# Kernel optimization log

Measured on AMD Instinct MI355X. Metric: run time of the kernel, lower is better.

Reference implementation:

```python
import jax, jax.numpy as jnp
import numpy as np

EPS = 1e-12  # matches torch F.normalize default eps


def _normalize(x):
    n = jnp.linalg.norm(x, axis=-1, keepdims=True)
    return x / jnp.maximum(n, EPS)


def _time_interp(t, e, L, E):
    """linear_interpolation_time: [B] t,e; L:[m] landmarks; E:[m,m] emb table."""
    m = L.shape[0]
    idx = jnp.searchsorted(L, t)              # torch.searchsorted, side='left'
    idx = jnp.where(idx == 0, 1, idx)
    idx = jnp.where(idx == m, m - 1, idx)
    E_hi, E_lo = E[idx], E[idx - 1]           # [B, m]
    L_hi, L_lo = L[idx], L[idx - 1]           # [B]
    coef = (E_hi - E_lo) / (L_hi - L_lo)[:, None]
    out = E_lo + coef * (t - L_lo)[:, None]
    # censor mask row i: mean of landmark embeddings j >= idx[i]
    denom = (m - idx).astype(E.dtype)[:, None]
    mask = (jnp.arange(m)[None, :] >= idx[:, None]).astype(E.dtype) / denom  # [B, m]
    out_censor = mask @ E.T                   # [B, m]
    e = e[:, None]
    return (out * e + out_censor * (1.0 - e)).astype(jnp.float32)


def setup_inputs() -> dict:
    key = jax.random.key(0)
    B, m = 8192, 256
    k_z, k_t, k_e = jax.random.split(key, 3)
    z = jax.random.normal(k_z, (B, m), dtype=jnp.float32)
    t = jax.random.uniform(k_t, (B,), dtype=jnp.float32, minval=0.0, maxval=10.0)
    e = (jax.random.uniform(k_e, (B,)) < 0.7).astype(jnp.float32)
    log_tau = jnp.zeros((1,), dtype=jnp.float32)            # tau=1.0 -> log 1 = 0
    time_landmark = jnp.linspace(0.0, 10.0, m, dtype=jnp.float32)
    time_emb_landmark = jnp.eye(m, dtype=jnp.float32)        # learnable eye init
    return {"z": z, "t": t, "e": e, "log_tau": log_tau,
            "time_emb_landmark": time_emb_landmark, "time_landmark": time_landmark}


def reference(z, t, e, log_tau, time_emb_landmark, time_landmark):
    B = z.shape[0]
    tau = jnp.sqrt(jnp.exp(log_tau))                         # [1]
    hz = _normalize(z) / tau                                  # enc = Identity
    hy = _normalize(_time_interp(t, e, time_landmark, time_emb_landmark)) / tau
    sim = hz @ hy.T                                           # [B, B]
    g = jnp.diagonal(sim)[:, None]                            # positives [B,1]
    # off-diagonal logits g0 - g: mask diagonal with -inf (exp -> 0 in logsumexp)
    eye = jnp.eye(B, dtype=bool)
    logits = jnp.where(eye, -jnp.inf, sim - g)
    slogits = jax.nn.logsumexp(logits, axis=1, keepdims=True)  # [B,1]
    # CrossEntropyLoss(sim, arange) per row = logsumexp(sim) - sim[i,i]
    dummy_ce = (jax.nn.logsumexp(sim, axis=1, keepdims=True) - g) - jnp.log(
        jnp.float32(B))
    out = jax.lax.stop_gradient(dummy_ce) + jnp.exp(
        slogits - jax.lax.stop_gradient(slogits)) - 1.0
    return jnp.clip(out, -5.0, 15.0)                          # [B,1]
```

## Files before the change

kernel.cpp:

```cpp
#include <hip/hip_runtime.h>
#include <hip/hip_bf16.h>

using short8 = __attribute__((ext_vector_type(8))) short;
using f32x4  = __attribute__((ext_vector_type(4))) float;

#define BM 128
#define BN 128
#define BK 64

__device__ inline void gload_lds16(const void* g, void* lds) {
    __builtin_amdgcn_global_load_lds(
        (const __attribute__((address_space(1))) void*)g,
        (__attribute__((address_space(3))) void*)lds, 16, 0, 0);
}

__global__ __launch_bounds__(256) void suffix_kernel(const float* __restrict__ E,
                                                     float* __restrict__ ST, int m) {
    int j = blockIdx.x;
    int k = threadIdx.x;
    int lane = k & 63, w = k >> 6;
    __shared__ float wtot[4];
    float v = (k < m) ? E[(size_t)j * m + k] : 0.f;
    #pragma unroll
    for (int off = 1; off < 64; off <<= 1) {
        float o = __shfl_down(v, off);
        if (lane + off < 64) v += o;
    }
    if (lane == 0) wtot[w] = v;
    __syncthreads();
    float add = 0.f;
    #pragma unroll
    for (int w2 = 0; w2 < 4; ++w2)
        if (w2 > w) add += wtot[w2];
    v += add;
    if (k < m) ST[(size_t)k * m + j] = v;
}

__global__ __launch_bounds__(256) void prep_kernel(
    const float* __restrict__ z, const float* __restrict__ t,
    const float* __restrict__ e, const float* __restrict__ log_tau,
    const float* __restrict__ E, const float* __restrict__ L,
    const float* __restrict__ ST,
    __hip_bfloat16* __restrict__ hz, __hip_bfloat16* __restrict__ hy,
    float* __restrict__ g, float* __restrict__ acc, int B, int m)
{
    int row  = blockIdx.x * 4 + (threadIdx.x >> 6);
    int lane = threadIdx.x & 63;
    if (row >= B) return;

    float tv = t[row], ev = e[row];

    int lo = 0, hi = m;
    while (lo < hi) { int mid = (lo + hi) >> 1; if (L[mid] < tv) lo = mid + 1; else hi = mid; }
    int idx = lo;
    if (idx == 0) idx = 1;
    if (idx == m) idx = m - 1;

    float Llo = L[idx - 1], Lhi = L[idx];
    float w    = (tv - Llo) / (Lhi - Llo);
    float invd = 1.0f / (float)(m - idx);
    float tau  = sqrtf(expf(log_tau[0]));
    float invtau = 1.0f / tau;

    int j0 = lane * 4;
    f32x4 zz = *(const f32x4*)&z[(size_t)row * m + j0];
    f32x4 El = *(const f32x4*)&E[(size_t)(idx - 1) * m + j0];
    f32x4 Eh = *(const f32x4*)&E[(size_t)idx * m + j0];
    f32x4 Sc = *(const f32x4*)&ST[(size_t)idx * m + j0];

    float yv[4];
    float ssy = 0.f, ssz = 0.f;
    #pragma unroll
    for (int p = 0; p < 4; ++p) {
        float yint = El[p] + (Eh[p] - El[p]) * w;
        float ycen = Sc[p] * invd;
        float y = yint * ev + ycen * (1.f - ev);
        yv[p] = y; ssy += y * y;
        ssz += zz[p] * zz[p];
    }
    #pragma unroll
    for (int off = 1; off < 64; off <<= 1) {
        ssy += __shfl_xor(ssy, off);
        ssz += __shfl_xor(ssz, off);
    }
    float sy = invtau / fmaxf(sqrtf(ssy), 1e-12f);
    float sz = invtau / fmaxf(sqrtf(ssz), 1e-12f);

    float gp = 0.f;
    ushort uy[4], uz[4];
    #pragma unroll
    for (int p = 0; p < 4; ++p) {
        float hyv = yv[p] * sy, hzv = zz[p] * sz;
        gp += hyv * hzv;
        __hip_bfloat16 hb = __float2bfloat16(hyv);
        __hip_bfloat16 zb = __float2bfloat16(hzv);
        uy[p] = *reinterpret_cast<unsigned short*>(&hb);
        uz[p] = *reinterpret_cast<unsigned short*>(&zb);
    }
    *(ushort4*)&hy[(size_t)row * m + j0] = make_ushort4(uy[0], uy[1], uy[2], uy[3]);
    *(ushort4*)&hz[(size_t)row * m + j0] = make_ushort4(uz[0], uz[1], uz[2], uz[3]);
    #pragma unroll
    for (int off = 1; off < 64; off <<= 1) gp += __shfl_xor(gp, off);
    if (lane == 0) { g[row] = gp; acc[row] = 0.f; }
}

__global__ __launch_bounds__(256, 2) void gemm_lse_kernel(
    const __hip_bfloat16* __restrict__ hz, const __hip_bfloat16* __restrict__ hy,
    float* __restrict__ row_acc, int B, int K)
{
    __shared__ __hip_bfloat16 As[2][BM * BK];
    __shared__ __hip_bfloat16 Bs[2][BN * BK];

    const int tid  = threadIdx.x;
    const int wv   = tid >> 6;
    const int lane = tid & 63;
    const int wr   = wv >> 1;
    const int wc   = wv & 1;

    int bx = blockIdx.x, by = blockIdx.y;
    {
        int nx = gridDim.x, ny = gridDim.y;
        int nwg = nx * ny;
        if ((nwg & 7) == 0 && ny >= 8) {
            int orig = by * nx + bx;
            int xcd = orig & 7;
            int pos = orig >> 3;
            by = (xcd << 3) | (pos & 7);
            bx = pos >> 3;
        }
    }
    const int row0 = by * BM;
    const int col0 = bx * BN;

    f32x4 acc[4][4];
    #pragma unroll
    for (int i = 0; i < 4; ++i)
        #pragma unroll
        for (int j = 0; j < 4; ++j)
            acc[i][j] = (f32x4){0.f, 0.f, 0.f, 0.f};

    const int l8 = lane >> 3;
    const int c8 = lane & 7;

    const int nkb = K / BK;

#define STAGE(buf, kb)                                                          \
    do {                                                                        \
        _Pragma("unroll")                                                       \
        for (int p = 0; p < 4; ++p) {                                           \
            int r  = p * 32 + wv * 8 + l8;                                      \
            int cg = c8 ^ (r & 7);                                              \
            gload_lds16(hz + (size_t)(row0 + r) * K + (kb) * BK + cg * 8,       \
                        (void*)&As[buf][(p * 32 + wv * 8) * BK]);               \
            gload_lds16(hy + (size_t)(col0 + r) * K + (kb) * BK + cg * 8,       \
                        (void*)&Bs[buf][(p * 32 + wv * 8) * BK]);               \
        }                                                                       \
    } while (0)

    STAGE(0, 0);

    for (int kb = 0; kb < nkb; ++kb) {
        const int cur = kb & 1;
        asm volatile("" ::: "memory");
        if (kb + 1 < nkb) {
            STAGE(cur ^ 1, kb + 1);
            asm volatile("s_waitcnt vmcnt(8)" ::: "memory");
        } else {
            asm volatile("s_waitcnt vmcnt(0)" ::: "memory");
        }
        __builtin_amdgcn_s_barrier();

        const int lm = lane & 15, lk = lane >> 4;
        #pragma unroll
        for (int kk = 0; kk < 2; ++kk) {
            short8 a[4], b[4];
            #pragma unroll
            for (int mi = 0; mi < 4; ++mi) {
                int rt = wr * 64 + mi * 16 + lm;
                int cs = (kk * 4 + lk) ^ (rt & 7);
                a[mi] = *(const short8*)&As[cur][rt * BK + cs * 8];
            }
            #pragma unroll
            for (int ni = 0; ni < 4; ++ni) {
                int rt = wc * 64 + ni * 16 + lm;
                int cs = (kk * 4 + lk) ^ (rt & 7);
                b[ni] = *(const short8*)&Bs[cur][rt * BK + cs * 8];
            }
            #pragma unroll
            for (int mi = 0; mi < 4; ++mi)
                #pragma unroll
                for (int ni = 0; ni < 4; ++ni)
                    acc[mi][ni] = __builtin_amdgcn_mfma_f32_16x16x32_bf16(
                        a[mi], b[ni], acc[mi][ni], 0, 0, 0);
        }
        __builtin_amdgcn_s_barrier();
    }
#undef STAGE

    const int lm = lane & 15, lg = lane >> 4;
    #pragma unroll
    for (int mi = 0; mi < 4; ++mi) {
        float rs[4] = {0.f, 0.f, 0.f, 0.f};
        #pragma unroll
        for (int ni = 0; ni < 4; ++ni) {
            #pragma unroll
            for (int r = 0; r < 4; ++r) rs[r] += __expf(acc[mi][ni][r]);
        }
        #pragma unroll
        for (int r = 0; r < 4; ++r) {
            float s = rs[r];
            s += __shfl_xor(s, 1);
            s += __shfl_xor(s, 2);
            s += __shfl_xor(s, 4);
            s += __shfl_xor(s, 8);
            if (lm == 0)
                unsafeAtomicAdd(&row_acc[row0 + wr * 64 + mi * 16 + lg * 4 + r], s);
        }
    }
}

__global__ void finalize_kernel(const float* __restrict__ acc, const float* __restrict__ g,
                                float* __restrict__ out, int B) {
    int i = blockIdx.x * 256 + threadIdx.x;
    if (i < B) {
        float v = logf(acc[i]) - g[i] - logf((float)B);
        out[i] = fminf(fmaxf(v, -5.f), 15.f);
    }
}

extern "C" void kernel_launch(void* const* d_in, const int* in_sizes, int n_in,
                              void* d_out, int out_size, void* d_ws, size_t ws_size,
                              hipStream_t stream) {
    const float* z       = (const float*)d_in[0];
    const float* t       = (const float*)d_in[1];
    const float* e       = (const float*)d_in[2];
    const float* log_tau = (const float*)d_in[3];
    const float* E       = (const float*)d_in[4];
    const float* L       = (const float*)d_in[5];
    float* out = (float*)d_out;

    const int B = in_sizes[1];
    const int m = in_sizes[5];

    char* w = (char*)d_ws;
    __hip_bfloat16* hz = (__hip_bfloat16*)w;
    __hip_bfloat16* hy = hz + (size_t)B * m;
    float* ST  = (float*)(hy + (size_t)B * m);
    float* g   = ST + (size_t)m * m;
    float* acc = g + B;

    suffix_kernel<<<m, 256, 0, stream>>>(E, ST, m);
    prep_kernel<<<B / 4, 256, 0, stream>>>(z, t, e, log_tau, E, L, ST, hz, hy, g, acc, B, m);
    dim3 grid2(B / BN, B / BM);
    gemm_lse_kernel<<<grid2, 256, 0, stream>>>(hz, hy, acc, B, m);
    finalize_kernel<<<(B + 255) / 256, 256, 0, stream>>>(acc, g, out, B);
}
```

Measured before the change: 141.8 us.

## Enlarge GEMM tile to 256x256 with 8 waves and interleaved staged prefetch

```diff
diff --git a/kernel.cpp b/kernel.cpp
--- a/kernel.cpp
+++ b/kernel.cpp
@@ -4,9 +4,10 @@
 using short8 = __attribute__((ext_vector_type(8))) short;
 using f32x4  = __attribute__((ext_vector_type(4))) float;
 
-#define BM 128
-#define BN 128
+#define BM 256
+#define BN 256
 #define BK 64
+#define NKT 4
 
 __device__ inline void gload_lds16(const void* g, void* lds) {
     __builtin_amdgcn_global_load_lds(
@@ -104,102 +105,137 @@
     if (lane == 0) { g[row] = gp; acc[row] = 0.f; }
 }
 
-__global__ __launch_bounds__(256, 2) void gemm_lse_kernel(
+__global__ __launch_bounds__(512, 2) void gemm_lse_kernel(
     const __hip_bfloat16* __restrict__ hz, const __hip_bfloat16* __restrict__ hy,
-    float* __restrict__ row_acc, int B, int K)
+    float* __restrict__ row_acc, int Brows, int K)
 {
     __shared__ __hip_bfloat16 As[2][BM * BK];
     __shared__ __hip_bfloat16 Bs[2][BN * BK];
 
     const int tid  = threadIdx.x;
-    const int wv   = tid >> 6;
+    const int wid  = tid >> 6;
     const int lane = tid & 63;
-    const int wr   = wv >> 1;
-    const int wc   = wv & 1;
+    const int wm   = wid >> 2;
+    const int wn   = wid & 3;
 
     int bx = blockIdx.x, by = blockIdx.y;
-    {
-        int nx = gridDim.x, ny = gridDim.y;
-        int nwg = nx * ny;
-        if ((nwg & 7) == 0 && ny >= 8) {
-            int orig = by * nx + bx;
-            int xcd = orig & 7;
-            int pos = orig >> 3;
-            by = (xcd << 3) | (pos & 7);
-            bx = pos >> 3;
-        }
-    }
-    const int row0 = by * BM;
-    const int col0 = bx * BN;
-
-    f32x4 acc[4][4];
-    #pragma unroll
-    for (int i = 0; i < 4; ++i)
+    if (gridDim.x == 32 && gridDim.y == 32) {
+        int orig = by * 32 + bx;
+        int xcd = orig & 7, pos = orig >> 3;
+        by = (xcd << 2) | (pos & 3);
+        bx = pos >> 2;
+    }
+    const int row0 = by * BM, col0 = bx * BN;
+
+    f32x4 acc[8][4];
+    #pragma unroll
+    for (int i = 0; i < 8; ++i)
         #pragma unroll
         for (int j = 0; j < 4; ++j)
             acc[i][j] = (f32x4){0.f, 0.f, 0.f, 0.f};
 
-    const int l8 = lane >> 3;
-    const int c8 = lane & 7;
-
-    const int nkb = K / BK;
-
-#define STAGE(buf, kb)                                                          \
+    const int srow = tid >> 3;
+    const int c8   = tid & 7;
+    const int cg   = c8 ^ (srow & 7);
+    const int lm   = lane & 15, lk = lane >> 4;
+
+#define STAGE_A(buf, kt)                                                        \
     do {                                                                        \
         _Pragma("unroll")                                                       \
-        for (int p = 0; p < 4; ++p) {                                           \
-            int r  = p * 32 + wv * 8 + l8;                                      \
-            int cg = c8 ^ (r & 7);                                              \
-            gload_lds16(hz + (size_t)(row0 + r) * K + (kb) * BK + cg * 8,       \
-                        (void*)&As[buf][(p * 32 + wv * 8) * BK]);               \
-            gload_lds16(hy + (size_t)(col0 + r) * K + (kb) * BK + cg * 8,       \
-                        (void*)&Bs[buf][(p * 32 + wv * 8) * BK]);               \
-        }                                                                       \
+        for (int s = 0; s < 4; ++s)                                             \
+            gload_lds16(hz + (size_t)(row0 + s * 64 + srow) * K + (kt) * BK + cg * 8, \
+                        (void*)&As[buf][s * 4096 + wid * 512]);                 \
     } while (0)
-
-    STAGE(0, 0);
-
-    for (int kb = 0; kb < nkb; ++kb) {
-        const int cur = kb & 1;
-        asm volatile("" ::: "memory");
-        if (kb + 1 < nkb) {
-            STAGE(cur ^ 1, kb + 1);
-            asm volatile("s_waitcnt vmcnt(8)" ::: "memory");
-        } else {
-            asm volatile("s_waitcnt vmcnt(0)" ::: "memory");
-        }
-        __builtin_amdgcn_s_barrier();
-
-        const int lm = lane & 15, lk = lane >> 4;
-        #pragma unroll
-        for (int kk = 0; kk < 2; ++kk) {
-            short8 a[4], b[4];
-            #pragma unroll
-            for (int mi = 0; mi < 4; ++mi) {
-                int rt = wr * 64 + mi * 16 + lm;
-                int cs = (kk * 4 + lk) ^ (rt & 7);
-                a[mi] = *(const short8*)&As[cur][rt * BK + cs * 8];
-            }
-            #pragma unroll
-            for (int ni = 0; ni < 4; ++ni) {
-                int rt = wc * 64 + ni * 16 + lm;
-                int cs = (kk * 4 + lk) ^ (rt & 7);
-                b[ni] = *(const short8*)&Bs[cur][rt * BK + cs * 8];
-            }
-            #pragma unroll
-            for (int mi = 0; mi < 4; ++mi)
-                #pragma unroll
-                for (int ni = 0; ni < 4; ++ni)
-                    acc[mi][ni] = __builtin_amdgcn_mfma_f32_16x16x32_bf16(
-                        a[mi], b[ni], acc[mi][ni], 0, 0, 0);
-        }
-        __builtin_amdgcn_s_barrier();
-    }
-#undef STAGE
-
-    const int lm = lane & 15, lg = lane >> 4;
-    #pragma unroll
-    for (int mi = 0; mi < 4; ++mi) {
+#define STAGE_B(buf, kt)                                                        \
+    do {                                                                        \
+        _Pragma("unroll")                                                       \
+        for (int s = 0; s < 4; ++s)                                             \
+            gload_lds16(hy + (size_t)(col0 + s * 64 + srow) * K + (kt) * BK + cg * 8, \
+                        (void*)&Bs[buf][s * 4096 + wid * 512]);                 \
+    } while (0)
+
+#define LDSA(buf, rt, q) (*(const short8*)&As[buf][(rt) * BK + ((q) ^ ((rt) & 7)) * 8])
+#define LDSB(buf, rt, q) (*(const short8*)&Bs[buf][(rt) * BK + ((q) ^ ((rt) & 7)) * 8])
+
+    STAGE_A(0, 0);
+    STAGE_B(0, 0);
+    asm volatile("s_waitcnt vmcnt(0)" ::: "memory");
+    __builtin_amdgcn_s_barrier();
+
+    #pragma unroll
+    for (int kt = 0; kt < NKT; ++kt) {
+        const int cur = kt & 1, nxt = cur ^ 1;
+        short8 a[4], b[4];
+
+        #pragma unroll
+        for (int mi = 0; mi < 4; ++mi)
+            a[mi] = LDSA(cur, wm * 128 + mi * 16 + lm, lk);
+        #pragma unroll
+        for (int ni = 0; ni < 4; ++ni)
+            b[ni] = LDSB(cur, wn * 64 + ni * 16 + lm, lk);
+        if (kt + 1 < NKT) STAGE_A(nxt, kt + 1);
+        __builtin_amdgcn_s_barrier();
+        __builtin_amdgcn_s_setprio(1);
+        #pragma unroll
+        for (int mi = 0; mi < 4; ++mi)
+            #pragma unroll
+            for (int ni = 0; ni < 4; ++ni)
+                acc[mi][ni] = __builtin_amdgcn_mfma_f32_16x16x32_bf16(a[mi], b[ni], acc[mi][ni], 0, 0, 0);
+        __builtin_amdgcn_s_setprio(0);
+        __builtin_amdgcn_s_barrier();
+
+        #pragma unroll
+        for (int mi = 0; mi < 4; ++mi)
+            a[mi] = LDSA(cur, wm * 128 + 64 + mi * 16 + lm, lk);
+        if (kt + 1 < NKT) STAGE_B(nxt, kt + 1);
+        __builtin_amdgcn_s_barrier();
+        __builtin_amdgcn_s_setprio(1);
+        #pragma unroll
+        for (int mi = 0; mi < 4; ++mi)
+            #pragma unroll
+            for (int ni = 0; ni < 4; ++ni)
+                acc[4 + mi][ni] = __builtin_amdgcn_mfma_f32_16x16x32_bf16(a[mi], b[ni], acc[4 + mi][ni], 0, 0, 0);
+        __builtin_amdgcn_s_setprio(0);
+        __builtin_amdgcn_s_barrier();
+
+        #pragma unroll
+        for (int mi = 0; mi < 4; ++mi)
+            a[mi] = LDSA(cur, wm * 128 + mi * 16 + lm, 4 + lk);
+        #pragma unroll
+        for (int ni = 0; ni < 4; ++ni)
+            b[ni] = LDSB(cur, wn * 64 + ni * 16 + lm, 4 + lk);
+        __builtin_amdgcn_s_barrier();
+        __builtin_amdgcn_s_setprio(1);
+        #pragma unroll
+        for (int mi = 0; mi < 4; ++mi)
+            #pragma unroll
+            for (int ni = 0; ni < 4; ++ni)
+                acc[mi][ni] = __builtin_amdgcn_mfma_f32_16x16x32_bf16(a[mi], b[ni], acc[mi][ni], 0, 0, 0);
+        __builtin_amdgcn_s_setprio(0);
+        __builtin_amdgcn_s_barrier();
+
+        #pragma unroll
+        for (int mi = 0; mi < 4; ++mi)
+            a[mi] = LDSA(cur, wm * 128 + 64 + mi * 16 + lm, 4 + lk);
+        __builtin_amdgcn_s_barrier();
+        __builtin_amdgcn_s_setprio(1);
+        #pragma unroll
+        for (int mi = 0; mi < 4; ++mi)
+            #pragma unroll
+            for (int ni = 0; ni < 4; ++ni)
+                acc[4 + mi][ni] = __builtin_amdgcn_mfma_f32_16x16x32_bf16(a[mi], b[ni], acc[4 + mi][ni], 0, 0, 0);
+        __builtin_amdgcn_s_setprio(0);
+        asm volatile("s_waitcnt vmcnt(0)" ::: "memory");
+        __builtin_amdgcn_s_barrier();
+    }
+#undef STAGE_A
+#undef STAGE_B
+#undef LDSA
+#undef LDSB
+
+    const int lg = lane >> 4;
+    #pragma unroll
+    for (int mi = 0; mi < 8; ++mi) {
         float rs[4] = {0.f, 0.f, 0.f, 0.f};
         #pragma unroll
         for (int ni = 0; ni < 4; ++ni) {
@@ -214,7 +250,7 @@
             s += __shfl_xor(s, 4);
             s += __shfl_xor(s, 8);
             if (lm == 0)
-                unsafeAtomicAdd(&row_acc[row0 + wr * 64 + mi * 16 + lg * 4 + r], s);
+                unsafeAtomicAdd(&row_acc[row0 + wm * 128 + mi * 16 + lg * 4 + r], s);
         }
     }
 }
@@ -252,6 +288,6 @@
     suffix_kernel<<<m, 256, 0, stream>>>(E, ST, m);
     prep_kernel<<<B / 4, 256, 0, stream>>>(z, t, e, log_tau, E, L, ST, hz, hy, g, acc, B, m);
     dim3 grid2(B / BN, B / BM);
-    gemm_lse_kernel<<<grid2, 256, 0, stream>>>(hz, hy, acc, B, m);
+    gemm_lse_kernel<<<grid2, 512, 0, stream>>>(hz, hy, acc, B, m);
     finalize_kernel<<<(B + 255) / 256, 256, 0, stream>>>(acc, g, out, B);
 }
```

New measurement: 135.1 us. -4.7%, faster.
